# Kernel optimization log

Hardware: AMD Instinct MI355X
Metric: run time of the kernel (lower is better)

## Reference

```python
import jax, jax.numpy as jnp
import numpy as np

N, E, T, Q, G = 50000, 800000, 1000000, 1000000, 4096
L, H, D, HID, ED = 3, 8, 16, 128, 16
EPS = 1e-8


def setup_inputs() -> dict:
    key = jax.random.key(0)
    ks = jax.random.split(key, 20)
    inp = {
        "x": jax.random.normal(ks[0], (N, HID), jnp.float32),
        "pos": jax.random.normal(ks[1], (N, 3), jnp.float32),
        "edge_attr": jax.random.normal(ks[2], (E, ED), jnp.float32),
        "temps": jax.random.uniform(ks[3], (G, 1), jnp.float32),
        "edge_index": jax.random.randint(ks[4], (2, E), 0, N, jnp.int32),
        "triple_index": jax.random.randint(ks[5], (3, T), 0, N, jnp.int32),
        "quadra_index": jax.random.randint(ks[6], (4, Q), 0, N, jnp.int32),
        "batch": jnp.sort(jax.random.randint(ks[7], (N,), 0, G, jnp.int32)),
        "W": jax.random.normal(ks[8], (L, HID, HID), jnp.float32) * 0.08,
        "a_e": jax.random.normal(ks[9], (L, H, 2 * D + 1), jnp.float32) * 0.1,
        "a_t": jax.random.normal(ks[10], (L, H, 2 * D + 1), jnp.float32) * 0.1,
        "a_q": jax.random.normal(ks[11], (L, H, 2 * D + 1), jnp.float32) * 0.1,
        "We": jax.random.normal(ks[12], (L, ED, H), jnp.float32) * 0.1,
        "W1": jax.random.normal(ks[13], (2 * HID + 1, 256), jnp.float32) * 0.06,
        "b1": jnp.zeros((256,), jnp.float32),
        "W2": jax.random.normal(ks[14], (256, 256), jnp.float32) * 0.06,
        "b2": jnp.zeros((256,), jnp.float32),
        "W3": jax.random.normal(ks[15], (256, 1), jnp.float32) * 0.06,
        "b3": jnp.zeros((1,), jnp.float32),
    }
    return inp


def _seg_softmax(logits, seg, n):
    # numerically stable segment softmax over destination nodes
    m = jax.ops.segment_max(logits, seg, num_segments=n)
    m = jnp.where(jnp.isfinite(m), m, 0.0)
    e = jnp.exp(logits - m[seg])
    s = jax.ops.segment_sum(e, seg, num_segments=n)
    return e / (s[seg] + 1e-16)


def _hop(hh, src, dst, geom, a, bias=None):
    # hh: [N,H,D]; gather-attend-scatter for one interaction order
    q, k = hh[dst], hh[src]                      # [M,H,D]
    logits = jnp.einsum('mhd,hd->mh', q, a[:, :D]) \
           + jnp.einsum('mhd,hd->mh', k, a[:, D:2 * D]) \
           + geom[:, None] * a[:, 2 * D]
    if bias is not None:
        logits = logits + bias
    logits = jax.nn.leaky_relu(logits, 0.2)
    alpha = _seg_softmax(logits, dst, hh.shape[0])  # [M,H]
    return jax.ops.segment_sum(k * alpha[..., None], dst, num_segments=hh.shape[0])


def _geom_features(pos, edge_index, triple_index, quadra_index):
    # edge distance
    d = jnp.linalg.norm(pos[edge_index[0]] - pos[edge_index[1]] + EPS, axis=-1)
    # triple angle cos at center node j of (i,j,k)
    i, j, k = triple_index
    u, v = pos[i] - pos[j], pos[k] - pos[j]
    cos_a = (u * v).sum(-1) / (jnp.linalg.norm(u, axis=-1) * jnp.linalg.norm(v, axis=-1) + EPS)
    # quadra dihedral cos of (p0,p1,p2,p3)
    p0, p1, p2, p3 = pos[quadra_index[0]], pos[quadra_index[1]], pos[quadra_index[2]], pos[quadra_index[3]]
    b1, b2, b3 = p1 - p0, p2 - p1, p3 - p2
    n1, n2 = jnp.cross(b1, b2), jnp.cross(b2, b3)
    cos_d = (n1 * n2).sum(-1) / (jnp.linalg.norm(n1, axis=-1) * jnp.linalg.norm(n2, axis=-1) + EPS)
    return d, cos_a, cos_d


def reference(x, pos, edge_attr, temps, edge_index, triple_index, quadra_index, batch,
              W, a_e, a_t, a_q, We, W1, b1, W2, b2, W3, b3):
    d, cos_a, cos_d = _geom_features(pos, edge_index, triple_index, quadra_index)
    e_src, e_dst = edge_index[1], edge_index[0]
    t_src, t_dst = triple_index[2], triple_index[0]
    q_src, q_dst = quadra_index[3], quadra_index[0]
    h = x
    for l in range(L):
        hl = h @ W[l]                              # [N,HID]
        hh = hl.reshape(N, H, D)
        bias_e = edge_attr @ We[l]                 # [E,H]
        agg = _hop(hh, e_src, e_dst, d, a_e[l], bias_e) \
            + _hop(hh, t_src, t_dst, cos_a, a_t[l]) \
            + _hop(hh, q_src, q_dst, cos_d, a_q[l])
        h = jax.nn.elu(hl + agg.reshape(N, HID))
    # readout: sum + max pooling per graph, concat temperature scalar
    s = jax.ops.segment_sum(h, batch, num_segments=G)
    mx = jax.ops.segment_max(h, batch, num_segments=G)
    mx = jnp.where(jnp.isfinite(mx), mx, 0.0)
    mol = jnp.concatenate([s, mx, temps], axis=-1)  # [G, 2*HID+1]
    hdn = jax.nn.elu(mol @ W1 + b1)
    hdn = jax.nn.elu(hdn @ W2 + b2)
    return hdn @ W3 + b3
```

## Files before the change

### kernel.cpp

```cpp
#include <hip/hip_runtime.h>
#include <hip/hip_fp16.h>

#define NN 50000
#define EE 800000
#define TT 1000000
#define QQ 1000000
#define GG 4096
#define HID 128
#define NH 8
#define DH 16
#define CAPC 96

typedef unsigned int u32;
typedef unsigned int u32x4 __attribute__((ext_vector_type(4)));

__device__ __forceinline__ float eluf(float x){ return x > 0.f ? x : expm1f(x); }

__device__ __forceinline__ u32 pack_sg(int src, float g){
  return ((u32)src << 16) | (u32)__half_as_ushort(__float2half(g));
}

__global__ void k_count3(const int* __restrict__ ei, const int* __restrict__ ti, const int* __restrict__ qi,
                         int* __restrict__ cnt){
  int i = blockIdx.x*blockDim.x + threadIdx.x;
  if (i < EE) atomicAdd(&cnt[ei[i]], 1);
  else if (i < EE+TT) atomicAdd(&cnt[NN + ti[i-EE]], 1);
  else if (i < EE+TT+QQ) atomicAdd(&cnt[2*NN + qi[i-EE-TT]], 1);
}

__global__ __launch_bounds__(1024) void k_scan4(const int* __restrict__ cnt,
    int* __restrict__ off_e, int* __restrict__ off_t, int* __restrict__ off_q,
    int* __restrict__ cur_e, int* __restrict__ cur_t, int* __restrict__ cur_q,
    const int* __restrict__ batch, int* __restrict__ goff){
  int b = blockIdx.x, t = threadIdx.x;
  if (b == 3){
    for (int g=t; g<=GG; g+=1024){
      int lo=0, hi=NN;
      while (lo<hi){ int mid=(lo+hi)>>1; if (batch[mid]<g) lo=mid+1; else hi=mid; }
      goff[g]=lo;
    }
    return;
  }
  __shared__ int part[1024];
  const int* c = cnt + b*NN;
  int* off = (b==0)?off_e:(b==1)?off_t:off_q;
  int* cur = (b==0)?cur_e:(b==1)?cur_t:cur_q;
  int chunk = (NN + 1023) >> 10;
  int s0 = t*chunk, s1 = min(NN, s0+chunk);
  int sum = 0;
  for (int i=s0;i<s1;i++) sum += c[i];
  part[t] = sum;
  __syncthreads();
  for (int d=1; d<1024; d<<=1){
    int v = (t>=d) ? part[t-d] : 0;
    __syncthreads();
    part[t] += v;
    __syncthreads();
  }
  int run = (t==0) ? 0 : part[t-1];
  for (int i=s0;i<s1;i++){ off[i]=run; cur[i]=run; run += c[i]; }
  if (t==0) off[NN] = part[1023];
}

__global__ void k_fillgeom(const float* __restrict__ pos, const float* __restrict__ edge_attr,
    const int* __restrict__ ei, const int* __restrict__ ti, const int* __restrict__ qi,
    int* __restrict__ cur_e, int* __restrict__ cur_t, int* __restrict__ cur_q,
    u32* __restrict__ csg_e, u32* __restrict__ csg_t, u32* __restrict__ csg_q,
    __half* __restrict__ eaP){
  int i = blockIdx.x*blockDim.x + threadIdx.x;
  if (i < EE){
    int dn = ei[i], sn = ei[EE+i];
    float dx = pos[dn*3+0]-pos[sn*3+0]+1e-8f;
    float dy = pos[dn*3+1]-pos[sn*3+1]+1e-8f;
    float dz = pos[dn*3+2]-pos[sn*3+2]+1e-8f;
    float d = sqrtf(dx*dx+dy*dy+dz*dz);
    int p = atomicAdd(&cur_e[dn], 1);
    __builtin_nontemporal_store(pack_sg(sn, d), &csg_e[p]);
    const float4* s = (const float4*)(edge_attr + (size_t)i*16);
    float4 v0=s[0], v1=s[1], v2=s[2], v3=s[3];
    __half2 h0=__floats2half2_rn(v0.x,v0.y), h1=__floats2half2_rn(v0.z,v0.w);
    __half2 h2=__floats2half2_rn(v1.x,v1.y), h3=__floats2half2_rn(v1.z,v1.w);
    __half2 h4=__floats2half2_rn(v2.x,v2.y), h5=__floats2half2_rn(v2.z,v2.w);
    __half2 h6=__floats2half2_rn(v3.x,v3.y), h7=__floats2half2_rn(v3.z,v3.w);
    u32x4 pk0, pk1;
    pk0[0]=*(u32*)&h0; pk0[1]=*(u32*)&h1; pk0[2]=*(u32*)&h2; pk0[3]=*(u32*)&h3;
    pk1[0]=*(u32*)&h4; pk1[1]=*(u32*)&h5; pk1[2]=*(u32*)&h6; pk1[3]=*(u32*)&h7;
    u32x4* dsts = (u32x4*)(eaP + (size_t)p*16);
    __builtin_nontemporal_store(pk0, &dsts[0]);
    __builtin_nontemporal_store(pk1, &dsts[1]);
  } else if (i < EE+TT){
    int m = i-EE;
    int a = ti[m], b = ti[TT+m], c = ti[2*TT+m];
    float ux = pos[a*3+0]-pos[b*3+0], uy = pos[a*3+1]-pos[b*3+1], uz = pos[a*3+2]-pos[b*3+2];
    float vx = pos[c*3+0]-pos[b*3+0], vy = pos[c*3+1]-pos[b*3+1], vz = pos[c*3+2]-pos[b*3+2];
    float num = ux*vx+uy*vy+uz*vz;
    float den = sqrtf(ux*ux+uy*uy+uz*uz)*sqrtf(vx*vx+vy*vy+vz*vz) + 1e-8f;
    int p = atomicAdd(&cur_t[a], 1);
    __builtin_nontemporal_store(pack_sg(c, num/den), &csg_t[p]);
  } else if (i < EE+TT+QQ){
    int m = i-EE-TT;
    int p0 = qi[m], p1 = qi[QQ+m], p2 = qi[2*QQ+m], p3 = qi[3*QQ+m];
    float b1x = pos[p1*3+0]-pos[p0*3+0], b1y = pos[p1*3+1]-pos[p0*3+1], b1z = pos[p1*3+2]-pos[p0*3+2];
    float b2x = pos[p2*3+0]-pos[p1*3+0], b2y = pos[p2*3+1]-pos[p1*3+1], b2z = pos[p2*3+2]-pos[p1*3+2];
    float b3x = pos[p3*3+0]-pos[p2*3+0], b3y = pos[p3*3+1]-pos[p2*3+1], b3z = pos[p3*3+2]-pos[p2*3+2];
    float n1x = b1y*b2z - b1z*b2y, n1y = b1z*b2x - b1x*b2z, n1z = b1x*b2y - b1y*b2x;
    float n2x = b2y*b3z - b2z*b3y, n2y = b2z*b3x - b2x*b3z, n2z = b2x*b3y - b2y*b3x;
    float num = n1x*n2x+n1y*n2y+n1z*n2z;
    float den = sqrtf(n1x*n1x+n1y*n1y+n1z*n1z)*sqrtf(n2x*n2x+n2y*n2y+n2z*n2z) + 1e-8f;
    int p = atomicAdd(&cur_q[p0], 1);
    __builtin_nontemporal_store(pack_sg(p3, num/den), &csg_q[p]);
  }
}

#define GR 16
__global__ __launch_bounds__(128) void k_gemm(const float* __restrict__ A, const float* __restrict__ W,
                                              __half* __restrict__ B16){
  int col = threadIdx.x;
  int r0 = blockIdx.x * GR;
  const float* Ab = A + (size_t)r0*HID;
  float acc[GR];
  #pragma unroll
  for (int r=0;r<GR;r++) acc[r]=0.f;
  #pragma unroll 4
  for (int k=0;k<HID;k++){
    float wv = W[k*HID+col];
    #pragma unroll
    for (int r=0;r<GR;r++) acc[r] = fmaf(Ab[r*HID+k], wv, acc[r]);
  }
  #pragma unroll
  for (int r=0;r<GR;r++) B16[(size_t)(r0+r)*HID+col] = __float2half(acc[r]);
}

__global__ void k_projbias(const __half* __restrict__ hl16,
    const float* __restrict__ ae, const float* __restrict__ at, const float* __restrict__ aq,
    const __half* __restrict__ eaP, const float* __restrict__ Wel,
    float* __restrict__ qa_e, float* __restrict__ ka_e,
    float* __restrict__ qa_t, float* __restrict__ ka_t,
    float* __restrict__ qa_q, float* __restrict__ ka_q,
    __half* __restrict__ biasP){
  int i = blockIdx.x*blockDim.x + threadIdx.x;
  if (i < NN*NH){
    int h = i & 7; int n = i >> 3;
    const __half2* v2 = (const __half2*)(hl16 + (size_t)n*HID + h*DH);
    float x[DH];
    #pragma unroll
    for (int d2=0; d2<8; d2++){ float2 f = __half22float2(v2[d2]); x[2*d2]=f.x; x[2*d2+1]=f.y; }
    const float* Ae = ae + h*33; const float* At_ = at + h*33; const float* Aq = aq + h*33;
    float s0=0,s1=0,s2=0,s3=0,s4=0,s5=0;
    #pragma unroll
    for (int d=0; d<DH; d++){
      s0 = fmaf(x[d], Ae[d],      s0);  s1 = fmaf(x[d], Ae[DH+d],  s1);
      s2 = fmaf(x[d], At_[d],     s2);  s3 = fmaf(x[d], At_[DH+d], s3);
      s4 = fmaf(x[d], Aq[d],      s4);  s5 = fmaf(x[d], Aq[DH+d],  s5);
    }
    qa_e[i]=s0; ka_e[i]=s1; qa_t[i]=s2; ka_t[i]=s3; qa_q[i]=s4; ka_q[i]=s5;
  } else {
    int m = i - NN*NH;
    if (m < EE){
      const __half2* s2 = (const __half2*)(eaP + (size_t)m*16);
      float a[16];
      #pragma unroll
      for (int d2=0; d2<8; d2++){ float2 f = __half22float2(s2[d2]); a[2*d2]=f.x; a[2*d2+1]=f.y; }
      __half2* bp = (__half2*)(biasP + (size_t)m*NH);
      #pragma unroll
      for (int hp=0; hp<4; hp++){
        float sa = 0.f, sb = 0.f;
        #pragma unroll
        for (int c=0;c<16;c++){
          sa = fmaf(a[c], Wel[c*NH + 2*hp],     sa);
          sb = fmaf(a[c], Wel[c*NH + 2*hp + 1], sb);
        }
        bp[hp] = __floats2half2_rn(sa, sb);
      }
    }
  }
}

__device__ __forceinline__ void gather_acc(const __half* __restrict__ hh16,
    const int* __restrict__ srcs, const float* __restrict__ es,
    int cnt, int w, int hg, int l, float& a0, float& a1){
  int m = w;
  for (; m+8 <= cnt; m += 8){
    int s0=srcs[m], s1=srcs[m+2], s2=srcs[m+4], s3=srcs[m+6];
    float e0=es[m*NH+hg], e1=es[(m+2)*NH+hg], e2=es[(m+4)*NH+hg], e3=es[(m+6)*NH+hg];
    float2 f0 = __half22float2(*(const __half2*)&hh16[(size_t)s0*HID + 2*l]);
    float2 f1 = __half22float2(*(const __half2*)&hh16[(size_t)s1*HID + 2*l]);
    float2 f2 = __half22float2(*(const __half2*)&hh16[(size_t)s2*HID + 2*l]);
    float2 f3 = __half22float2(*(const __half2*)&hh16[(size_t)s3*HID + 2*l]);
    a0 = fmaf(f0.x, e0, a0); a1 = fmaf(f0.y, e0, a1);
    a0 = fmaf(f1.x, e1, a0); a1 = fmaf(f1.y, e1, a1);
    a0 = fmaf(f2.x, e2, a0); a1 = fmaf(f2.y, e2, a1);
    a0 = fmaf(f3.x, e3, a0); a1 = fmaf(f3.y, e3, a1);
  }
  for (; m < cnt; m += 2){
    int s0 = srcs[m];
    float e0 = es[m*NH+hg];
    float2 f0 = __half22float2(*(const __half2*)&hh16[(size_t)s0*HID + 2*l]);
    a0 = fmaf(f0.x, e0, a0); a1 = fmaf(f0.y, e0, a1);
  }
}

__global__ __launch_bounds__(128) void k_hop3(
    const int* __restrict__ off_e, const int* __restrict__ off_t, const int* __restrict__ off_q,
    const u32* __restrict__ csg_e, const u32* __restrict__ csg_t, const u32* __restrict__ csg_q,
    const __half* __restrict__ biasP,
    const float* __restrict__ qa_e, const float* __restrict__ ka_e,
    const float* __restrict__ qa_t, const float* __restrict__ ka_t,
    const float* __restrict__ qa_q, const float* __restrict__ ka_q,
    const float* __restrict__ ae, const float* __restrict__ at, const float* __restrict__ aq,
    const __half* __restrict__ hh16, const __half* __restrict__ hlr16, float* __restrict__ hout){
  __shared__ float sh_e[3][CAPC*NH];
  __shared__ int   sh_src[3][CAPC];
  __shared__ float sh_geom[3][CAPC];
  __shared__ float sh_s[3*NH];
  __shared__ float sh_qa[3*NH];
  __shared__ float sh_coef[3*NH];
  int n = blockIdx.x, t = threadIdx.x;
  int w = t >> 6, l = t & 63;
  if (t < 24){
    int p = t>>3, h = t&7;
    const float* a  = (p==0)?ae:(p==1)?at:aq;
    const float* qa = (p==0)?qa_e:(p==1)?qa_t:qa_q;
    sh_coef[t] = a[h*33+32];
    sh_qa[t]   = qa[n*NH+h];
    sh_s[t]    = 0.f;
  }
  int st_e = off_e[n], de = off_e[n+1]-st_e;
  int st_t = off_t[n], dt = off_t[n+1]-st_t;
  int st_q = off_q[n], dq = off_q[n+1]-st_q;
  __syncthreads();
  float aE0=0,aE1=0,aT0=0,aT1=0,aQ0=0,aQ1=0;
  int h  = t & 7;
  int hg = l >> 3;
  int maxd = max(de, max(dt, dq));
  for (int base=0; base<maxd; base+=CAPC){
    int ce = min(CAPC, de-base); if (ce<0) ce=0;
    int ct = min(CAPC, dt-base); if (ct<0) ct=0;
    int cq = min(CAPC, dq-base); if (cq<0) cq=0;
    if (t < ce){ u32 v = csg_e[st_e+base+t]; sh_src[0][t]=(int)(v>>16); sh_geom[0][t]=__half2float(__ushort_as_half((unsigned short)(v&0xFFFFu))); }
    if (t < ct){ u32 v = csg_t[st_t+base+t]; sh_src[1][t]=(int)(v>>16); sh_geom[1][t]=__half2float(__ushort_as_half((unsigned short)(v&0xFFFFu))); }
    if (t < cq){ u32 v = csg_q[st_q+base+t]; sh_src[2][t]=(int)(v>>16); sh_geom[2][t]=__half2float(__ushort_as_half((unsigned short)(v&0xFFFFu))); }
    __syncthreads();
    float dE=0.f, dT=0.f, dQ=0.f;
    for (int i=t; i<ce*NH; i+=128){
      int m = i>>3;
      float lg = sh_qa[h] + ka_e[sh_src[0][m]*NH+h] + sh_geom[0][m]*sh_coef[h]
               + __half2float(biasP[(size_t)(st_e+base)*NH + i]);
      lg = lg>=0.f ? lg : 0.2f*lg;
      float e = __expf(lg);
      sh_e[0][i] = e; dE += e;
    }
    for (int i=t; i<ct*NH; i+=128){
      int m = i>>3;
      float lg = sh_qa[8+h] + ka_t[sh_src[1][m]*NH+h] + sh_geom[1][m]*sh_coef[8+h];
      lg = lg>=0.f ? lg : 0.2f*lg;
      float e = __expf(lg);
      sh_e[1][i] = e; dT += e;
    }
    for (int i=t; i<cq*NH; i+=128){
      int m = i>>3;
      float lg = sh_qa[16+h] + ka_q[sh_src[2][m]*NH+h] + sh_geom[2][m]*sh_coef[16+h];
      lg = lg>=0.f ? lg : 0.2f*lg;
      float e = __expf(lg);
      sh_e[2][i] = e; dQ += e;
    }
    dE += __shfl_xor(dE, 8); dE += __shfl_xor(dE, 16); dE += __shfl_xor(dE, 32);
    dT += __shfl_xor(dT, 8); dT += __shfl_xor(dT, 16); dT += __shfl_xor(dT, 32);
    dQ += __shfl_xor(dQ, 8); dQ += __shfl_xor(dQ, 16); dQ += __shfl_xor(dQ, 32);
    if (l < 8){
      atomicAdd(&sh_s[l], dE);
      atomicAdd(&sh_s[8+l], dT);
      atomicAdd(&sh_s[16+l], dQ);
    }
    __syncthreads();
    gather_acc(hh16, sh_src[0], sh_e[0], ce, w, hg, l, aE0, aE1);
    gather_acc(hh16, sh_src[1], sh_e[1], ct, w, hg, l, aT0, aT1);
    gather_acc(hh16, sh_src[2], sh_e[2], cq, w, hg, l, aQ0, aQ1);
    __syncthreads();
  }
  float* red = &sh_e[0][0];
  *(float2*)&red[(0*2+w)*128 + 2*l] = make_float2(aE0, aE1);
  *(float2*)&red[(1*2+w)*128 + 2*l] = make_float2(aT0, aT1);
  *(float2*)&red[(2*2+w)*128 + 2*l] = make_float2(aQ0, aQ1);
  __syncthreads();
  int ho = t >> 4;
  float outv = (red[t]       + red[128+t]) / (sh_s[ho]    + 1e-16f)
             + (red[256+t]   + red[384+t]) / (sh_s[8+ho]  + 1e-16f)
             + (red[512+t]   + red[640+t]) / (sh_s[16+ho] + 1e-16f);
  size_t oi = (size_t)n*HID + t;
  hout[oi] = eluf(__half2float(hlr16[oi]) + outv);
}

__global__ __launch_bounds__(128) void k_pool(const float* __restrict__ h, const int* __restrict__ goff,
                                              float* __restrict__ gs, float* __restrict__ gmx){
  int g = blockIdx.x, t = threadIdx.x;
  int s = goff[g], e = goff[g+1];
  float sum = 0.f, mx = -INFINITY;
  for (int n=s; n<e; n++){
    float v = h[(size_t)n*HID+t];
    sum += v; mx = fmaxf(mx, v);
  }
  gs[(size_t)g*HID+t] = sum;
  gmx[(size_t)g*HID+t] = (s < e) ? mx : 0.f;
}

#define GPB 8
#define MSTR 260
__global__ __launch_bounds__(256) void k_mlp(const float* __restrict__ gs, const float* __restrict__ gmx,
    const float* __restrict__ temps,
    const float* __restrict__ W1, const float* __restrict__ b1,
    const float* __restrict__ W2, const float* __restrict__ b2,
    const float* __restrict__ W3, const float* __restrict__ b3,
    float* __restrict__ out){
  __shared__ float mol[GPB][MSTR];
  __shared__ float hd[GPB][MSTR];
  int g0 = blockIdx.x*GPB, t = threadIdx.x;
  for (int i=t; i<GPB*HID; i+=256){
    int g=i>>7, d=i&127;
    mol[g][d]     = gs[(size_t)(g0+g)*HID+d];
    mol[g][128+d] = gmx[(size_t)(g0+g)*HID+d];
  }
  if (t < GPB){ mol[t][256]=temps[g0+t]; mol[t][257]=0.f; mol[t][258]=0.f; mol[t][259]=0.f; }
  __syncthreads();
  float acc[GPB];
  #pragma unroll
  for (int g=0;g<GPB;g++) acc[g]=b1[t];
  for (int k0=0;k0<256;k0+=4){
    float w0=W1[(size_t)(k0+0)*256+t], w1=W1[(size_t)(k0+1)*256+t];
    float w2=W1[(size_t)(k0+2)*256+t], w3=W1[(size_t)(k0+3)*256+t];
    #pragma unroll
    for (int g=0;g<GPB;g++){
      float4 m4 = *(const float4*)&mol[g][k0];
      acc[g] = fmaf(m4.x,w0, fmaf(m4.y,w1, fmaf(m4.z,w2, fmaf(m4.w,w3, acc[g]))));
    }
  }
  { float wl=W1[(size_t)256*256+t];
    #pragma unroll
    for (int g=0;g<GPB;g++) acc[g]=fmaf(mol[g][256],wl,acc[g]); }
  #pragma unroll
  for (int g=0;g<GPB;g++) hd[g][t]=eluf(acc[g]);
  __syncthreads();
  #pragma unroll
  for (int g=0;g<GPB;g++) acc[g]=b2[t];
  for (int k0=0;k0<256;k0+=4){
    float w0=W2[(size_t)(k0+0)*256+t], w1=W2[(size_t)(k0+1)*256+t];
    float w2=W2[(size_t)(k0+2)*256+t], w3=W2[(size_t)(k0+3)*256+t];
    #pragma unroll
    for (int g=0;g<GPB;g++){
      float4 h4 = *(const float4*)&hd[g][k0];
      acc[g] = fmaf(h4.x,w0, fmaf(h4.y,w1, fmaf(h4.z,w2, fmaf(h4.w,w3, acc[g]))));
    }
  }
  float w3v = W3[t];
  #pragma unroll
  for (int g=0;g<GPB;g++) mol[g][t] = eluf(acc[g])*w3v;
  __syncthreads();
  int g = t >> 5, j = t & 31;
  float s = 0.f;
  for (int i=j; i<256; i+=32) s += mol[g][i];
  #pragma unroll
  for (int d=16; d>0; d>>=1) s += __shfl_down(s, d, 32);
  if (j == 0) out[g0+g] = s + b3[0];
}

extern "C" void kernel_launch(void* const* d_in, const int* in_sizes, int n_in,
                              void* d_out, int out_size, void* d_ws, size_t ws_size,
                              hipStream_t stream){
  const float* x         = (const float*)d_in[0];
  const float* pos       = (const float*)d_in[1];
  const float* edge_attr = (const float*)d_in[2];
  const float* temps     = (const float*)d_in[3];
  const int*   ei        = (const int*)d_in[4];
  const int*   ti        = (const int*)d_in[5];
  const int*   qi        = (const int*)d_in[6];
  const int*   batch     = (const int*)d_in[7];
  const float* W         = (const float*)d_in[8];
  const float* a_e       = (const float*)d_in[9];
  const float* a_t       = (const float*)d_in[10];
  const float* a_q       = (const float*)d_in[11];
  const float* We        = (const float*)d_in[12];
  const float* W1        = (const float*)d_in[13];
  const float* b1        = (const float*)d_in[14];
  const float* W2        = (const float*)d_in[15];
  const float* b2        = (const float*)d_in[16];
  const float* W3        = (const float*)d_in[17];
  const float* b3        = (const float*)d_in[18];
  float* out = (float*)d_out;

  char* base = (char*)d_ws; size_t woff = 0;
  auto alloc = [&](size_t bytes)->void*{
    void* p = base + woff;
    woff = (woff + bytes + 255) & ~(size_t)255;
    return p;
  };
  float*  hbuf   = (float*)alloc((size_t)NN*HID*4);
  __half* hl16   = (__half*)alloc((size_t)NN*HID*2);
  float*  qa_e   = (float*)alloc((size_t)NN*NH*4);
  float*  ka_e   = (float*)alloc((size_t)NN*NH*4);
  float*  qa_t   = (float*)alloc((size_t)NN*NH*4);
  float*  ka_t   = (float*)alloc((size_t)NN*NH*4);
  float*  qa_q   = (float*)alloc((size_t)NN*NH*4);
  float*  ka_q   = (float*)alloc((size_t)NN*NH*4);
  u32*    csg_e  = (u32*)alloc((size_t)EE*4);
  u32*    csg_t  = (u32*)alloc((size_t)TT*4);
  u32*    csg_q  = (u32*)alloc((size_t)QQ*4);
  __half* eaP    = (__half*)alloc((size_t)EE*16*2);
  __half* biasP  = (__half*)alloc((size_t)EE*NH*2);
  float*  gs     = (float*)alloc((size_t)GG*HID*4);
  float*  gmx    = (float*)alloc((size_t)GG*HID*4);
  int*    cnt    = (int*)alloc((size_t)3*NN*4);
  int*    off_e  = (int*)alloc((size_t)(NN+1)*4);
  int*    off_t  = (int*)alloc((size_t)(NN+1)*4);
  int*    off_q  = (int*)alloc((size_t)(NN+1)*4);
  int*    cur_e  = (int*)alloc((size_t)NN*4);
  int*    cur_t  = (int*)alloc((size_t)NN*4);
  int*    cur_q  = (int*)alloc((size_t)NN*4);
  int*    goff   = (int*)alloc((size_t)(GG+1)*4);

  hipMemsetAsync(cnt, 0, (size_t)3*NN*4, stream);
  int tot = EE+TT+QQ;
  k_count3<<<(tot+255)/256,256,0,stream>>>(ei, ti, qi, cnt);
  k_scan4<<<4,1024,0,stream>>>(cnt, off_e, off_t, off_q, cur_e, cur_t, cur_q, batch, goff);
  k_fillgeom<<<(tot+255)/256,256,0,stream>>>(pos, edge_attr, ei, ti, qi, cur_e, cur_t, cur_q,
                                             csg_e, csg_t, csg_q, eaP);

  for (int l=0; l<3; l++){
    const float* hin = (l==0) ? x : hbuf;
    k_gemm<<<NN/GR,128,0,stream>>>(hin, W + (size_t)l*HID*HID, hl16);
    k_projbias<<<(NN*NH+EE+255)/256,256,0,stream>>>(hl16, a_e+l*264, a_t+l*264, a_q+l*264,
                                                    eaP, We + l*DH*NH,
                                                    qa_e, ka_e, qa_t, ka_t, qa_q, ka_q, biasP);
    k_hop3<<<NN,128,0,stream>>>(off_e, off_t, off_q, csg_e, csg_t, csg_q, biasP,
                                qa_e, ka_e, qa_t, ka_t, qa_q, ka_q,
                                a_e+l*264, a_t+l*264, a_q+l*264,
                                hl16, hl16, hbuf);
  }

  k_pool<<<GG,128,0,stream>>>(hbuf, goff, gs, gmx);
  k_mlp<<<GG/GPB,256,0,stream>>>(gs, gmx, temps, W1, b1, W2, b2, W3, b3, out);
}
```

Measured before the change: 1.228 ms.

## Precompute edge biases for all layers once; bucket triple/quad CSR fill via staging

The edge bias projection edge_attr@We is now computed for all three layers in the CSR fill kernel. It is stored with the packed src/geom word in a 64-byte per-edge record, so the per-layer bias pass over E is removed. The triple and quad CSR fill becomes a two-pass bucketed scatter: tiles are sorted in shared memory by 256-node destination bucket and written to a staging buffer, then a second kernel places entries using local shared atomics. This aims to cut scattered global atomics and uncoalesced writes. The cost is an extra staging buffer and kernel launch, and hop3 now reads strided 64-byte records for its edge data.

```diff
diff --git a/kernel.cpp b/kernel.cpp
--- a/kernel.cpp
+++ b/kernel.cpp
@@ -10,6 +10,11 @@
 #define NH 8
 #define DH 16
 #define CAPC 96
+
+#define TILE 2048
+#define KPT 8
+#define NB 196
+#define NBG 392
 
 typedef unsigned int u32;
 typedef unsigned int u32x4 __attribute__((ext_vector_type(4)));
@@ -62,53 +67,145 @@
   if (t==0) off[NN] = part[1023];
 }
 
-__global__ void k_fillgeom(const float* __restrict__ pos, const float* __restrict__ edge_attr,
-    const int* __restrict__ ei, const int* __restrict__ ti, const int* __restrict__ qi,
-    int* __restrict__ cur_e, int* __restrict__ cur_t, int* __restrict__ cur_q,
-    u32* __restrict__ csg_e, u32* __restrict__ csg_t, u32* __restrict__ csg_q,
-    __half* __restrict__ eaP){
+__global__ void k_fillE(const float* __restrict__ pos, const float* __restrict__ edge_attr,
+    const int* __restrict__ ei, const float* __restrict__ We,
+    int* __restrict__ cur_e, u32* __restrict__ eRec){
   int i = blockIdx.x*blockDim.x + threadIdx.x;
-  if (i < EE){
-    int dn = ei[i], sn = ei[EE+i];
-    float dx = pos[dn*3+0]-pos[sn*3+0]+1e-8f;
-    float dy = pos[dn*3+1]-pos[sn*3+1]+1e-8f;
-    float dz = pos[dn*3+2]-pos[sn*3+2]+1e-8f;
-    float d = sqrtf(dx*dx+dy*dy+dz*dz);
-    int p = atomicAdd(&cur_e[dn], 1);
-    __builtin_nontemporal_store(pack_sg(sn, d), &csg_e[p]);
-    const float4* s = (const float4*)(edge_attr + (size_t)i*16);
-    float4 v0=s[0], v1=s[1], v2=s[2], v3=s[3];
-    __half2 h0=__floats2half2_rn(v0.x,v0.y), h1=__floats2half2_rn(v0.z,v0.w);
-    __half2 h2=__floats2half2_rn(v1.x,v1.y), h3=__floats2half2_rn(v1.z,v1.w);
-    __half2 h4=__floats2half2_rn(v2.x,v2.y), h5=__floats2half2_rn(v2.z,v2.w);
-    __half2 h6=__floats2half2_rn(v3.x,v3.y), h7=__floats2half2_rn(v3.z,v3.w);
-    u32x4 pk0, pk1;
-    pk0[0]=*(u32*)&h0; pk0[1]=*(u32*)&h1; pk0[2]=*(u32*)&h2; pk0[3]=*(u32*)&h3;
-    pk1[0]=*(u32*)&h4; pk1[1]=*(u32*)&h5; pk1[2]=*(u32*)&h6; pk1[3]=*(u32*)&h7;
-    u32x4* dsts = (u32x4*)(eaP + (size_t)p*16);
-    __builtin_nontemporal_store(pk0, &dsts[0]);
-    __builtin_nontemporal_store(pk1, &dsts[1]);
-  } else if (i < EE+TT){
-    int m = i-EE;
-    int a = ti[m], b = ti[TT+m], c = ti[2*TT+m];
-    float ux = pos[a*3+0]-pos[b*3+0], uy = pos[a*3+1]-pos[b*3+1], uz = pos[a*3+2]-pos[b*3+2];
-    float vx = pos[c*3+0]-pos[b*3+0], vy = pos[c*3+1]-pos[b*3+1], vz = pos[c*3+2]-pos[b*3+2];
-    float num = ux*vx+uy*vy+uz*vz;
-    float den = sqrtf(ux*ux+uy*uy+uz*uz)*sqrtf(vx*vx+vy*vy+vz*vz) + 1e-8f;
-    int p = atomicAdd(&cur_t[a], 1);
-    __builtin_nontemporal_store(pack_sg(c, num/den), &csg_t[p]);
-  } else if (i < EE+TT+QQ){
-    int m = i-EE-TT;
-    int p0 = qi[m], p1 = qi[QQ+m], p2 = qi[2*QQ+m], p3 = qi[3*QQ+m];
-    float b1x = pos[p1*3+0]-pos[p0*3+0], b1y = pos[p1*3+1]-pos[p0*3+1], b1z = pos[p1*3+2]-pos[p0*3+2];
-    float b2x = pos[p2*3+0]-pos[p1*3+0], b2y = pos[p2*3+1]-pos[p1*3+1], b2z = pos[p2*3+2]-pos[p1*3+2];
-    float b3x = pos[p3*3+0]-pos[p2*3+0], b3y = pos[p3*3+1]-pos[p2*3+1], b3z = pos[p3*3+2]-pos[p2*3+2];
-    float n1x = b1y*b2z - b1z*b2y, n1y = b1z*b2x - b1x*b2z, n1z = b1x*b2y - b1y*b2x;
-    float n2x = b2y*b3z - b2z*b3y, n2y = b2z*b3x - b2x*b3z, n2z = b2x*b3y - b2y*b3x;
-    float num = n1x*n2x+n1y*n2y+n1z*n2z;
-    float den = sqrtf(n1x*n1x+n1y*n1y+n1z*n1z)*sqrtf(n2x*n2x+n2y*n2y+n2z*n2z) + 1e-8f;
-    int p = atomicAdd(&cur_q[p0], 1);
-    __builtin_nontemporal_store(pack_sg(p3, num/den), &csg_q[p]);
+  if (i >= EE) return;
+  int dn = ei[i], sn = ei[EE+i];
+  float dx = pos[dn*3+0]-pos[sn*3+0]+1e-8f;
+  float dy = pos[dn*3+1]-pos[sn*3+1]+1e-8f;
+  float dz = pos[dn*3+2]-pos[sn*3+2]+1e-8f;
+  float d = sqrtf(dx*dx+dy*dy+dz*dz);
+  int p = atomicAdd(&cur_e[dn], 1);
+  const float4* s = (const float4*)(edge_attr + (size_t)i*16);
+  float4 v0=s[0], v1=s[1], v2=s[2], v3=s[3];
+  float a[16] = {v0.x,v0.y,v0.z,v0.w, v1.x,v1.y,v1.z,v1.w,
+                 v2.x,v2.y,v2.z,v2.w, v3.x,v3.y,v3.z,v3.w};
+  u32x4 r[4];
+  r[0][0] = pack_sg(sn, d); r[0][1]=0; r[0][2]=0; r[0][3]=0;
+  #pragma unroll
+  for (int l=0; l<3; l++){
+    const float* Wel = We + l*DH*NH;
+    #pragma unroll
+    for (int hp=0; hp<4; hp++){
+      float sa=0.f, sb=0.f;
+      #pragma unroll
+      for (int c=0;c<16;c++){
+        sa = fmaf(a[c], Wel[c*NH + 2*hp],     sa);
+        sb = fmaf(a[c], Wel[c*NH + 2*hp + 1], sb);
+      }
+      __half2 hh = __floats2half2_rn(sa, sb);
+      r[1+l][hp] = *(u32*)&hh;
+    }
+  }
+  u32x4* dst4 = (u32x4*)(eRec + (size_t)p*16);
+  dst4[0]=r[0]; dst4[1]=r[1]; dst4[2]=r[2]; dst4[3]=r[3];
+}
+
+__global__ __launch_bounds__(256) void k_fillTQ_A(const float* __restrict__ pos,
+    const int* __restrict__ ti, const int* __restrict__ qi,
+    const int* __restrict__ off_t, const int* __restrict__ off_q,
+    u32* __restrict__ gcur, uint2* __restrict__ stg){
+  __shared__ u32 s_sg[TILE];
+  __shared__ u32 s_dw[TILE];
+  __shared__ u32 s_cnt[NBG];
+  __shared__ u32 s_scan[512];
+  __shared__ u32 s_gb[NBG];
+  int t = threadIdx.x;
+  size_t tile0 = (size_t)blockIdx.x * TILE;
+  for (int i=t;i<NBG;i+=256) s_cnt[i]=0;
+  __syncthreads();
+  u32 my_sg[KPT], my_dw[KPT], my_rank[KPT]; int my_bg[KPT];
+  #pragma unroll
+  for (int k=0;k<KPT;k++){
+    size_t idx = tile0 + (size_t)k*256 + t;
+    my_bg[k] = -1;
+    if (idx < (size_t)TT+QQ){
+      int dst, src; float g;
+      int typeq = (idx >= (size_t)TT);
+      if (!typeq){
+        int m = (int)idx;
+        int ia=ti[m], jb=ti[TT+m], kc=ti[2*TT+m];
+        float ux=pos[ia*3+0]-pos[jb*3+0], uy=pos[ia*3+1]-pos[jb*3+1], uz=pos[ia*3+2]-pos[jb*3+2];
+        float vx=pos[kc*3+0]-pos[jb*3+0], vy=pos[kc*3+1]-pos[jb*3+1], vz=pos[kc*3+2]-pos[jb*3+2];
+        float num = ux*vx+uy*vy+uz*vz;
+        float den = sqrtf(ux*ux+uy*uy+uz*uz)*sqrtf(vx*vx+vy*vy+vz*vz) + 1e-8f;
+        g = num/den; dst = ia; src = kc;
+      } else {
+        int m = (int)(idx - TT);
+        int p0=qi[m], p1=qi[QQ+m], p2=qi[2*QQ+m], p3=qi[3*QQ+m];
+        float b1x=pos[p1*3+0]-pos[p0*3+0], b1y=pos[p1*3+1]-pos[p0*3+1], b1z=pos[p1*3+2]-pos[p0*3+2];
+        float b2x=pos[p2*3+0]-pos[p1*3+0], b2y=pos[p2*3+1]-pos[p1*3+1], b2z=pos[p2*3+2]-pos[p1*3+2];
+        float b3x=pos[p3*3+0]-pos[p2*3+0], b3y=pos[p3*3+1]-pos[p2*3+1], b3z=pos[p3*3+2]-pos[p2*3+2];
+        float n1x=b1y*b2z-b1z*b2y, n1y=b1z*b2x-b1x*b2z, n1z=b1x*b2y-b1y*b2x;
+        float n2x=b2y*b3z-b2z*b3y, n2y=b2z*b3x-b2x*b3z, n2z=b2x*b3y-b2y*b3x;
+        float num = n1x*n2x+n1y*n2y+n1z*n2z;
+        float den = sqrtf(n1x*n1x+n1y*n1y+n1z*n1z)*sqrtf(n2x*n2x+n2y*n2y+n2z*n2z) + 1e-8f;
+        g = num/den; dst = p0; src = p3;
+      }
+      int bg = (typeq?NB:0) + (dst>>8);
+      my_sg[k] = pack_sg(src, g);
+      my_dw[k] = (u32)dst | ((u32)typeq<<20);
+      my_bg[k] = bg;
+      my_rank[k] = atomicAdd(&s_cnt[bg], 1u);
+    }
+  }
+  __syncthreads();
+  int i0=t, i1=t+256;
+  s_scan[i0] = (i0<NBG)? s_cnt[i0] : 0u;
+  s_scan[i1] = (i1<NBG)? s_cnt[i1] : 0u;
+  __syncthreads();
+  for (int d=1; d<512; d<<=1){
+    u32 a0 = (i0>=d)? s_scan[i0-d] : 0u;
+    u32 a1 = (i1>=d)? s_scan[i1-d] : 0u;
+    __syncthreads();
+    s_scan[i0]+=a0; s_scan[i1]+=a1;
+    __syncthreads();
+  }
+  u32 total = s_scan[NBG-1];
+  #pragma unroll
+  for (int k=0;k<KPT;k++){
+    if (my_bg[k]>=0){
+      u32 slot = s_scan[my_bg[k]] - s_cnt[my_bg[k]] + my_rank[k];
+      s_sg[slot]=my_sg[k]; s_dw[slot]=my_dw[k];
+    }
+  }
+  for (int i=t;i<NBG;i+=256)
+    s_gb[i] = s_cnt[i] ? atomicAdd(&gcur[i], s_cnt[i]) : 0u;
+  __syncthreads();
+  for (u32 j=t; j<total; j+=256){
+    u32 dw = s_dw[j];
+    int typeq = (dw>>20)&1;
+    int dst = dw & 0xFFFFF;
+    int bg = (typeq?NB:0) + (dst>>8);
+    u32 rank = j - (s_scan[bg]-s_cnt[bg]);
+    int w0 = (typeq? bg-NB : bg)*256;
+    size_t sbase = typeq ? (size_t)TT + (size_t)off_q[w0] : (size_t)off_t[w0];
+    stg[sbase + s_gb[bg] + rank] = make_uint2(s_sg[j], dw);
+  }
+}
+
+__global__ __launch_bounds__(256) void k_fillTQ_B(const uint2* __restrict__ stg,
+    const int* __restrict__ off_t, const int* __restrict__ off_q,
+    u32* __restrict__ csg_t, u32* __restrict__ csg_q){
+  __shared__ int curL[256];
+  int b = blockIdx.x, t = threadIdx.x;
+  int typeq = (b>=NB);
+  int bl = typeq? b-NB : b;
+  const int* off = typeq? off_q : off_t;
+  u32* csg = typeq? csg_q : csg_t;
+  int w0 = bl*256, w1 = min(w0+256, NN);
+  int s0 = off[w0], s1 = off[w1];
+  for (int i=t; i<w1-w0; i+=256) curL[i] = off[w0+i];
+  __syncthreads();
+  size_t sb = (typeq? (size_t)TT : 0) + (size_t)s0;
+  int cnt = s1 - s0;
+  for (int i=t; i<cnt; i+=256){
+    uint2 r = stg[sb+i];
+    int dst = r.y & 0xFFFFF;
+    int p = atomicAdd(&curL[dst-w0], 1);
+    csg[p] = r.x;
   }
 }
 
@@ -131,49 +228,27 @@
   for (int r=0;r<GR;r++) B16[(size_t)(r0+r)*HID+col] = __float2half(acc[r]);
 }
 
-__global__ void k_projbias(const __half* __restrict__ hl16,
+__global__ void k_proj(const __half* __restrict__ hl16,
     const float* __restrict__ ae, const float* __restrict__ at, const float* __restrict__ aq,
-    const __half* __restrict__ eaP, const float* __restrict__ Wel,
     float* __restrict__ qa_e, float* __restrict__ ka_e,
     float* __restrict__ qa_t, float* __restrict__ ka_t,
-    float* __restrict__ qa_q, float* __restrict__ ka_q,
-    __half* __restrict__ biasP){
+    float* __restrict__ qa_q, float* __restrict__ ka_q){
   int i = blockIdx.x*blockDim.x + threadIdx.x;
-  if (i < NN*NH){
-    int h = i & 7; int n = i >> 3;
-    const __half2* v2 = (const __half2*)(hl16 + (size_t)n*HID + h*DH);
-    float x[DH];
-    #pragma unroll
-    for (int d2=0; d2<8; d2++){ float2 f = __half22float2(v2[d2]); x[2*d2]=f.x; x[2*d2+1]=f.y; }
-    const float* Ae = ae + h*33; const float* At_ = at + h*33; const float* Aq = aq + h*33;
-    float s0=0,s1=0,s2=0,s3=0,s4=0,s5=0;
-    #pragma unroll
-    for (int d=0; d<DH; d++){
-      s0 = fmaf(x[d], Ae[d],      s0);  s1 = fmaf(x[d], Ae[DH+d],  s1);
-      s2 = fmaf(x[d], At_[d],     s2);  s3 = fmaf(x[d], At_[DH+d], s3);
-      s4 = fmaf(x[d], Aq[d],      s4);  s5 = fmaf(x[d], Aq[DH+d],  s5);
-    }
-    qa_e[i]=s0; ka_e[i]=s1; qa_t[i]=s2; ka_t[i]=s3; qa_q[i]=s4; ka_q[i]=s5;
-  } else {
-    int m = i - NN*NH;
-    if (m < EE){
-      const __half2* s2 = (const __half2*)(eaP + (size_t)m*16);
-      float a[16];
-      #pragma unroll
-      for (int d2=0; d2<8; d2++){ float2 f = __half22float2(s2[d2]); a[2*d2]=f.x; a[2*d2+1]=f.y; }
-      __half2* bp = (__half2*)(biasP + (size_t)m*NH);
-      #pragma unroll
-      for (int hp=0; hp<4; hp++){
-        float sa = 0.f, sb = 0.f;
-        #pragma unroll
-        for (int c=0;c<16;c++){
-          sa = fmaf(a[c], Wel[c*NH + 2*hp],     sa);
-          sb = fmaf(a[c], Wel[c*NH + 2*hp + 1], sb);
-        }
-        bp[hp] = __floats2half2_rn(sa, sb);
-      }
-    }
-  }
+  if (i >= NN*NH) return;
+  int h = i & 7; int n = i >> 3;
+  const __half2* v2 = (const __half2*)(hl16 + (size_t)n*HID + h*DH);
+  float x[DH];
+  #pragma unroll
+  for (int d2=0; d2<8; d2++){ float2 f = __half22float2(v2[d2]); x[2*d2]=f.x; x[2*d2+1]=f.y; }
+  const float* Ae = ae + h*33; const float* At_ = at + h*33; const float* Aq = aq + h*33;
+  float s0=0,s1=0,s2=0,s3=0,s4=0,s5=0;
+  #pragma unroll
+  for (int d=0; d<DH; d++){
+    s0 = fmaf(x[d], Ae[d],      s0);  s1 = fmaf(x[d], Ae[DH+d],  s1);
+    s2 = fmaf(x[d], At_[d],     s2);  s3 = fmaf(x[d], At_[DH+d], s3);
+    s4 = fmaf(x[d], Aq[d],      s4);  s5 = fmaf(x[d], Aq[DH+d],  s5);
+  }
+  qa_e[i]=s0; ka_e[i]=s1; qa_t[i]=s2; ka_t[i]=s3; qa_q[i]=s4; ka_q[i]=s5;
 }
 
 __device__ __forceinline__ void gather_acc(const __half* __restrict__ hh16,
@@ -202,13 +277,14 @@
 
 __global__ __launch_bounds__(128) void k_hop3(
     const int* __restrict__ off_e, const int* __restrict__ off_t, const int* __restrict__ off_q,
-    const u32* __restrict__ csg_e, const u32* __restrict__ csg_t, const u32* __restrict__ csg_q,
-    const __half* __restrict__ biasP,
+    const u32* __restrict__ eRec,
+    const u32* __restrict__ csg_t, const u32* __restrict__ csg_q,
     const float* __restrict__ qa_e, const float* __restrict__ ka_e,
     const float* __restrict__ qa_t, const float* __restrict__ ka_t,
     const float* __restrict__ qa_q, const float* __restrict__ ka_q,
     const float* __restrict__ ae, const float* __restrict__ at, const float* __restrict__ aq,
-    const __half* __restrict__ hh16, const __half* __restrict__ hlr16, float* __restrict__ hout){
+    const __half* __restrict__ hh16, const __half* __restrict__ hlr16, float* __restrict__ hout,
+    int L){
   __shared__ float sh_e[3][CAPC*NH];
   __shared__ int   sh_src[3][CAPC];
   __shared__ float sh_geom[3][CAPC];
@@ -232,12 +308,13 @@
   float aE0=0,aE1=0,aT0=0,aT1=0,aQ0=0,aQ1=0;
   int h  = t & 7;
   int hg = l >> 3;
+  const __half* eRecH = (const __half*)eRec;
   int maxd = max(de, max(dt, dq));
   for (int base=0; base<maxd; base+=CAPC){
     int ce = min(CAPC, de-base); if (ce<0) ce=0;
     int ct = min(CAPC, dt-base); if (ct<0) ct=0;
     int cq = min(CAPC, dq-base); if (cq<0) cq=0;
-    if (t < ce){ u32 v = csg_e[st_e+base+t]; sh_src[0][t]=(int)(v>>16); sh_geom[0][t]=__half2float(__ushort_as_half((unsigned short)(v&0xFFFFu))); }
+    if (t < ce){ u32 v = eRec[(size_t)(st_e+base+t)*16]; sh_src[0][t]=(int)(v>>16); sh_geom[0][t]=__half2float(__ushort_as_half((unsigned short)(v&0xFFFFu))); }
     if (t < ct){ u32 v = csg_t[st_t+base+t]; sh_src[1][t]=(int)(v>>16); sh_geom[1][t]=__half2float(__ushort_as_half((unsigned short)(v&0xFFFFu))); }
     if (t < cq){ u32 v = csg_q[st_q+base+t]; sh_src[2][t]=(int)(v>>16); sh_geom[2][t]=__half2float(__ushort_as_half((unsigned short)(v&0xFFFFu))); }
     __syncthreads();
@@ -245,7 +322,7 @@
     for (int i=t; i<ce*NH; i+=128){
       int m = i>>3;
       float lg = sh_qa[h] + ka_e[sh_src[0][m]*NH+h] + sh_geom[0][m]*sh_coef[h]
-               + __half2float(biasP[(size_t)(st_e+base)*NH + i]);
+               + __half2float(eRecH[(size_t)(st_e+base+m)*32 + 8 + 8*L + h]);
       lg = lg>=0.f ? lg : 0.2f*lg;
       float e = __expf(lg);
       sh_e[0][i] = e; dE += e;
@@ -401,14 +478,14 @@
   float*  ka_t   = (float*)alloc((size_t)NN*NH*4);
   float*  qa_q   = (float*)alloc((size_t)NN*NH*4);
   float*  ka_q   = (float*)alloc((size_t)NN*NH*4);
-  u32*    csg_e  = (u32*)alloc((size_t)EE*4);
+  u32*    eRec   = (u32*)alloc((size_t)EE*64);
   u32*    csg_t  = (u32*)alloc((size_t)TT*4);
   u32*    csg_q  = (u32*)alloc((size_t)QQ*4);
-  __half* eaP    = (__half*)alloc((size_t)EE*16*2);
-  __half* biasP  = (__half*)alloc((size_t)EE*NH*2);
+  uint2*  stg    = (uint2*)alloc((size_t)(TT+QQ)*8);
   float*  gs     = (float*)alloc((size_t)GG*HID*4);
   float*  gmx    = (float*)alloc((size_t)GG*HID*4);
   int*    cnt    = (int*)alloc((size_t)3*NN*4);
+  u32*    gcur   = (u32*)alloc((size_t)NBG*4);
   int*    off_e  = (int*)alloc((size_t)(NN+1)*4);
   int*    off_t  = (int*)alloc((size_t)(NN+1)*4);
   int*    off_q  = (int*)alloc((size_t)(NN+1)*4);
@@ -418,22 +495,23 @@
   int*    goff   = (int*)alloc((size_t)(GG+1)*4);
 
   hipMemsetAsync(cnt, 0, (size_t)3*NN*4, stream);
+  hipMemsetAsync(gcur, 0, (size_t)NBG*4, stream);
   int tot = EE+TT+QQ;
   k_count3<<<(tot+255)/256,256,0,stream>>>(ei, ti, qi, cnt);
   k_scan4<<<4,1024,0,stream>>>(cnt, off_e, off_t, off_q, cur_e, cur_t, cur_q, batch, goff);
-  k_fillgeom<<<(tot+255)/256,256,0,stream>>>(pos, edge_attr, ei, ti, qi, cur_e, cur_t, cur_q,
-                                             csg_e, csg_t, csg_q, eaP);
+  k_fillE<<<(EE+255)/256,256,0,stream>>>(pos, edge_attr, ei, We, cur_e, eRec);
+  k_fillTQ_A<<<(TT+QQ+TILE-1)/TILE,256,0,stream>>>(pos, ti, qi, off_t, off_q, gcur, stg);
+  k_fillTQ_B<<<NBG,256,0,stream>>>(stg, off_t, off_q, csg_t, csg_q);
 
   for (int l=0; l<3; l++){
     const float* hin = (l==0) ? x : hbuf;
     k_gemm<<<NN/GR,128,0,stream>>>(hin, W + (size_t)l*HID*HID, hl16);
-    k_projbias<<<(NN*NH+EE+255)/256,256,0,stream>>>(hl16, a_e+l*264, a_t+l*264, a_q+l*264,
-                                                    eaP, We + l*DH*NH,
-                                                    qa_e, ka_e, qa_t, ka_t, qa_q, ka_q, biasP);
-    k_hop3<<<NN,128,0,stream>>>(off_e, off_t, off_q, csg_e, csg_t, csg_q, biasP,
+    k_proj<<<(NN*NH+255)/256,256,0,stream>>>(hl16, a_e+l*264, a_t+l*264, a_q+l*264,
+                                             qa_e, ka_e, qa_t, ka_t, qa_q, ka_q);
+    k_hop3<<<NN,128,0,stream>>>(off_e, off_t, off_q, eRec, csg_t, csg_q,
                                 qa_e, ka_e, qa_t, ka_t, qa_q, ka_q,
                                 a_e+l*264, a_t+l*264, a_q+l*264,
-                                hl16, hl16, hbuf);
+                                hl16, hl16, hbuf, l);
   }
 
   k_pool<<<GG,128,0,stream>>>(hbuf, goff, gs, gmx);
```

New measurement: 1.188 ms. 3.2% less time.
